# Kernel tuning notes

Measured on AMD Instinct MI355X. Metric: run time of the kernel, lower is better.

## Reference

```python
import jax, jax.numpy as jnp
import numpy as np

KERNEL_SIZE = 5
SIGMA_SPACE = 1.0
SIGMA_COLOR = 0.1
PAD = KERNEL_SIZE // 2


def make_spatial_kernel(kernel_size, sigma_space):
    r = kernel_size // 2
    coords = jnp.arange(-r, r + 1, dtype=jnp.float32)
    xx, yy = jnp.meshgrid(coords, coords, indexing='ij')
    return jnp.exp(-(xx ** 2 + yy ** 2) / (2.0 * sigma_space ** 2))  # [K, K]


def setup_inputs() -> dict:
    key = jax.random.key(0)
    x = jax.random.uniform(key, (4, 3, 512, 512), dtype=jnp.float32)
    spatial_kernel = make_spatial_kernel(KERNEL_SIZE, SIGMA_SPACE)
    sigma_color = jnp.float32(SIGMA_COLOR)
    return {"x": x, "spatial_kernel": spatial_kernel, "sigma_color": sigma_color}


def reference(x, spatial_kernel, sigma_color):
    # x: [B, C, H, W]; spatial_kernel: [K, K] (fixed buffer, computed at init)
    B, C, H, W = x.shape
    K = KERNEL_SIZE
    padded = jnp.pad(x, ((0, 0), (0, 0), (PAD, PAD), (PAD, PAD)), mode='reflect')
    # Gather KxK windows as a trailing tap axis: [B, C, H, W, K*K]
    patches = jnp.stack(
        [padded[:, :, i:i + H, j:j + W] for i in range(K) for j in range(K)],
        axis=-1,
    )
    sk = spatial_kernel.reshape(-1)  # [K*K]
    color_diff = patches - x[..., None]
    color_weight = jnp.exp(-(color_diff ** 2) / (2.0 * sigma_color ** 2))
    weight = sk * color_weight  # [B, C, H, W, K*K]
    weight = weight / (jnp.sum(weight, axis=-1, keepdims=True) + 1e-8)
    return jnp.sum(weight * patches, axis=-1)  # [B, C, H, W]
```

## Files before the change

kernel.cpp:

```cpp
#include <hip/hip_runtime.h>

#define KSIZE 5
#define PAD 2

__global__ __launch_bounds__(256) void bilateral_kernel(
    const float* __restrict__ x,
    const float* __restrict__ sk,
    const float* __restrict__ sigma_color,
    float* __restrict__ out,
    int H, int W, int total)
{
    __shared__ float s_sk[KSIZE * KSIZE];
    __shared__ float s_c2;

    int t = threadIdx.x;
    if (t < KSIZE * KSIZE) s_sk[t] = sk[t];
    if (t == KSIZE * KSIZE) {
        float sc = sigma_color[0];
        s_c2 = -1.4426950408889634f / (2.0f * sc * sc);
    }
    __syncthreads();

    int idx = blockIdx.x * 256 + t;
    if (idx >= total) return;

    int w = idx % W;
    int hw = idx / W;
    int h = hw % H;
    int plane = hw / H;
    int base = plane * H * W;

    float cx = x[idx];
    float c2 = s_c2;

    int hoff[KSIZE];
    int woff[KSIZE];
#pragma unroll
    for (int i = 0; i < KSIZE; ++i) {
        int hv = h + i - PAD;
        hv = (hv < 0) ? -hv : hv;
        hv = (hv >= H) ? (2 * H - 2 - hv) : hv;
        hoff[i] = hv * W;
    }
#pragma unroll
    for (int j = 0; j < KSIZE; ++j) {
        int wv = w + j - PAD;
        wv = (wv < 0) ? -wv : wv;
        wv = (wv >= W) ? (2 * W - 2 - wv) : wv;
        woff[j] = wv;
    }

    float wsum = 0.0f;
    float acc  = 0.0f;
#pragma unroll
    for (int i = 0; i < KSIZE; ++i) {
#pragma unroll
        for (int j = 0; j < KSIZE; ++j) {
            float p = x[base + hoff[i] + woff[j]];
            float d = p - cx;
            float wgt = s_sk[i * KSIZE + j] * __builtin_amdgcn_exp2f(d * d * c2);
            wsum += wgt;
            acc = fmaf(wgt, p, acc);
        }
    }

    out[idx] = acc * __builtin_amdgcn_rcpf(wsum + 1e-8f);
}

extern "C" void kernel_launch(void* const* d_in, const int* in_sizes, int n_in,
                              void* d_out, int out_size, void* d_ws, size_t ws_size,
                              hipStream_t stream) {
    const float* x  = (const float*)d_in[0];
    const float* sk = (const float*)d_in[1];
    const float* sc = (const float*)d_in[2];
    float* out = (float*)d_out;

    const int H = 512, W = 512;
    const int total = in_sizes[0];
    const int blocks = (total + 255) / 256;

    bilateral_kernel<<<blocks, 256, 0, stream>>>(x, sk, sc, out, H, W, total);
}
```

Measured before the change: 90.19 us.

## Compute four pixels per thread with register window and folded log spatial weights

Each thread now handles four consecutive pixels. It loads a 5x8 register window with vectorized float4 loads plus scalar halo loads, so neighbouring taps are reused instead of refetched 25 times per pixel. The spatial weight is folded into the exponent as log(sk) through an FMA, which removes a multiply per tap. Output is written as a float4, and the launch shrinks fourfold, which lowers parallelism and raises register pressure. Shapes are hardcoded to 512 and the tail guard is removed.

Result: faster. 85.30 us (-5.4%).

```diff
diff --git a/kernel.cpp b/kernel.cpp
--- a/kernel.cpp
+++ b/kernel.cpp
@@ -1,70 +1,85 @@
 #include <hip/hip_runtime.h>
 
-#define KSIZE 5
-#define PAD 2
+constexpr int H = 512, W = 512;
+constexpr int K = 5, PADR = 2;
 
 __global__ __launch_bounds__(256) void bilateral_kernel(
     const float* __restrict__ x,
     const float* __restrict__ sk,
     const float* __restrict__ sigma_color,
-    float* __restrict__ out,
-    int H, int W, int total)
+    float* __restrict__ out)
 {
-    __shared__ float s_sk[KSIZE * KSIZE];
+    __shared__ float s_lsk[K * K];
     __shared__ float s_c2;
 
     int t = threadIdx.x;
-    if (t < KSIZE * KSIZE) s_sk[t] = sk[t];
-    if (t == KSIZE * KSIZE) {
+    if (t < K * K) s_lsk[t] = __builtin_amdgcn_logf(sk[t]);
+    if (t == K * K) {
         float sc = sigma_color[0];
         s_c2 = -1.4426950408889634f / (2.0f * sc * sc);
     }
     __syncthreads();
 
-    int idx = blockIdx.x * 256 + t;
-    if (idx >= total) return;
-
-    int w = idx % W;
-    int hw = idx / W;
-    int h = hw % H;
-    int plane = hw / H;
-    int base = plane * H * W;
-
-    float cx = x[idx];
+    float lsk[K * K];
+#pragma unroll
+    for (int k = 0; k < K * K; ++k) lsk[k] = s_lsk[k];
     float c2 = s_c2;
 
-    int hoff[KSIZE];
-    int woff[KSIZE];
+    int gid = blockIdx.x * 256 + t;
+    int p0 = gid << 2;
+    int w0 = p0 & (W - 1);
+    int row = p0 >> 9;
+    int h = row & (H - 1);
+    int plane = row >> 9;
+    const float* xp = x + (size_t)plane * (H * W);
+
+    int hoff[K];
 #pragma unroll
-    for (int i = 0; i < KSIZE; ++i) {
-        int hv = h + i - PAD;
+    for (int i = 0; i < K; ++i) {
+        int hv = h + i - PADR;
         hv = (hv < 0) ? -hv : hv;
         hv = (hv >= H) ? (2 * H - 2 - hv) : hv;
-        hoff[i] = hv * W;
+        hoff[i] = hv << 9;
     }
+    int wl0 = w0 - 2; wl0 = (wl0 < 0) ? -wl0 : wl0;
+    int wl1 = w0 - 1; wl1 = (wl1 < 0) ? -wl1 : wl1;
+    int wr0 = w0 + 4; wr0 = (wr0 >= W) ? (2 * W - 2 - wr0) : wr0;
+    int wr1 = w0 + 5; wr1 = (wr1 >= W) ? (2 * W - 2 - wr1) : wr1;
+
+    float win[K][8];
 #pragma unroll
-    for (int j = 0; j < KSIZE; ++j) {
-        int wv = w + j - PAD;
-        wv = (wv < 0) ? -wv : wv;
-        wv = (wv >= W) ? (2 * W - 2 - wv) : wv;
-        woff[j] = wv;
+    for (int i = 0; i < K; ++i) {
+        const float* rp = xp + hoff[i];
+        float4 m = *(const float4*)(rp + w0);
+        win[i][2] = m.x; win[i][3] = m.y; win[i][4] = m.z; win[i][5] = m.w;
+        win[i][0] = rp[wl0];
+        win[i][1] = rp[wl1];
+        win[i][6] = rp[wr0];
+        win[i][7] = rp[wr1];
     }
 
-    float wsum = 0.0f;
-    float acc  = 0.0f;
+    float res[4];
 #pragma unroll
-    for (int i = 0; i < KSIZE; ++i) {
+    for (int p = 0; p < 4; ++p) {
+        float cx = win[2][p + 2];
+        float wsum = 0.0f, acc = 0.0f;
 #pragma unroll
-        for (int j = 0; j < KSIZE; ++j) {
-            float p = x[base + hoff[i] + woff[j]];
-            float d = p - cx;
-            float wgt = s_sk[i * KSIZE + j] * __builtin_amdgcn_exp2f(d * d * c2);
-            wsum += wgt;
-            acc = fmaf(wgt, p, acc);
+        for (int i = 0; i < K; ++i) {
+#pragma unroll
+            for (int j = 0; j < K; ++j) {
+                float v = win[i][p + j];
+                float d = v - cx;
+                float wgt = __builtin_amdgcn_exp2f(fmaf(d * c2, d, lsk[i * K + j]));
+                wsum += wgt;
+                acc = fmaf(wgt, v, acc);
+            }
         }
+        res[p] = acc * __builtin_amdgcn_rcpf(wsum + 1e-8f);
     }
 
-    out[idx] = acc * __builtin_amdgcn_rcpf(wsum + 1e-8f);
+    float4 o;
+    o.x = res[0]; o.y = res[1]; o.z = res[2]; o.w = res[3];
+    *(float4*)(out + p0) = o;
 }
 
 extern "C" void kernel_launch(void* const* d_in, const int* in_sizes, int n_in,
@@ -75,9 +90,7 @@
     const float* sc = (const float*)d_in[2];
     float* out = (float*)d_out;
 
-    const int H = 512, W = 512;
     const int total = in_sizes[0];
-    const int blocks = (total + 255) / 256;
-
-    bilateral_kernel<<<blocks, 256, 0, stream>>>(x, sk, sc, out, H, W, total);
+    const int blocks = total / (256 * 4);
+    bilateral_kernel<<<blocks, 256, 0, stream>>>(x, sk, sc, out);
 }
```
